# Kernel optimization log

Measured on AMD Instinct MI355X. Metric: run time of the kernel, lower is better.

Reference implementation:

```python
import jax, jax.numpy as jnp
import numpy as np

VOCAB = 100      # input_size == output_size
H = 2048         # hidden_size
NL = 2           # n_layers
SW = 256         # stack_width
SD = 200         # stack_depth
RIN = H + SW     # rnn_input_size (has_stack=True)


def _p(key, shape, fan_in):
    return jax.random.normal(key, shape, jnp.float32) / np.float32(np.sqrt(fan_in))


def setup_inputs() -> dict:
    key = jax.random.key(0)
    ks = jax.random.split(key, 12)
    return dict(
        inp=jax.random.randint(ks[0], (1,), 0, VOCAB),
        hidden=jax.random.normal(ks[1], (NL, 1, H), jnp.float32),
        stack=jax.random.normal(ks[2], (1, SD, SW), jnp.float32),
        emb=_p(ks[3], (VOCAB, H), H),
        Wc=_p(ks[4], (3, NL * H), NL * H), bc=jnp.zeros((3,), jnp.float32),
        Ws=_p(ks[5], (SW, NL * H), NL * H), bs=jnp.zeros((SW,), jnp.float32),
        Wih0=_p(ks[6], (3 * H, RIN), RIN), Whh0=_p(ks[7], (3 * H, H), H),
        bih0=jnp.zeros((3 * H,), jnp.float32), bhh0=jnp.zeros((3 * H,), jnp.float32),
        Wih1=_p(ks[8], (3 * H, H), H), Whh1=_p(ks[9], (3 * H, H), H),
        bih1=jnp.zeros((3 * H,), jnp.float32), bhh1=jnp.zeros((3 * H,), jnp.float32),
        Wd=_p(ks[10], (VOCAB, H), H), bd=jnp.zeros((VOCAB,), jnp.float32),
    )


def _gru_step(x, h, Wih, Whh, bih, bhh):
    # PyTorch GRU cell semantics. x: (1, in), h: (1, H)
    gi = x @ Wih.T + bih            # (1, 3H)
    gh = h @ Whh.T + bhh            # (1, 3H)
    i_r, i_z, i_n = jnp.split(gi, 3, axis=-1)
    h_r, h_z, h_n = jnp.split(gh, 3, axis=-1)
    r = jax.nn.sigmoid(i_r + h_r)
    z = jax.nn.sigmoid(i_z + h_z)
    n = jnp.tanh(i_n + r * h_n)
    return (1.0 - z) * n + z * h


def reference(inp, hidden, stack, emb, Wc, bc, Ws, bs,
              Wih0, Whh0, bih0, bhh0, Wih1, Whh1, bih1, bhh1, Wd, bd):
    # embedding: (1,) -> (1, 1, H)
    x_emb = emb[inp].reshape(1, 1, H)
    # hidden -> (1, NL*H) for stack control / stack input layers
    h2s = jnp.transpose(hidden, (1, 0, 2)).reshape(1, NL * H)
    controls = jax.nn.softmax(h2s @ Wc.T + bc, axis=1)      # (1, 3)
    s_in = jnp.tanh(h2s @ Ws.T + bs).reshape(1, 1, SW)      # (1, 1, SW)
    a_push = controls[0, 0]
    a_pop = controls[0, 1]
    a_noop = controls[0, 2]
    stack_up = jnp.concatenate([s_in, stack[:, :-1]], axis=1)
    stack_down = jnp.concatenate(
        [stack[:, 1:], jnp.zeros((1, 1, SW), stack.dtype)], axis=1)
    new_stack = a_noop * stack + a_push * stack_up + a_pop * stack_down
    # rnn input: concat embedding with stack top -> (1, H+SW)
    x = jnp.concatenate([x_emb, new_stack[:, :1, :]], axis=2)[0]
    h0 = _gru_step(x, hidden[0], Wih0, Whh0, bih0, bhh0)
    h1 = _gru_step(h0, hidden[1], Wih1, Whh1, bih1, bhh1)
    next_hidden = jnp.stack([h0, h1], axis=0)               # (NL, 1, H)
    logits = h1 @ Wd.T + bd                                 # (1, VOCAB)
    return logits, next_hidden, new_stack
```

## Files before the change

### kernel.cpp

```cpp
#include <hip/hip_runtime.h>
#include <hip/hip_bf16.h>

#define H 2048
#define RIN 2304
#define SW 256
#define SD 200

#define WS_CDOT 0
#define WS_SDOT 4
#define WS_GH0  260
#define WS_GH1  6404
#define WS_GI0  12548


typedef __attribute__((ext_vector_type(4))) float f32x4;

__device__ __forceinline__ float wave_reduce(float acc) {
  #pragma unroll
  for (int off = 32; off > 0; off >>= 1) acc += __shfl_down(acc, off);
  return acc;
}

__device__ __forceinline__ float dot2048_part(const float* __restrict__ w,
                                              const float* __restrict__ x) {
  int lane = threadIdx.x & 63;
  const f32x4* w4 = (const f32x4*)w + lane;
  const f32x4* x4 = (const f32x4*)x + lane;
  f32x4 a0 = w4[0],   a1 = w4[64],  a2 = w4[128], a3 = w4[192];
  f32x4 a4 = w4[256], a5 = w4[320], a6 = w4[384], a7 = w4[448];
  f32x4 b0 = x4[0],   b1 = x4[64],  b2 = x4[128], b3 = x4[192];
  f32x4 b4 = x4[256], b5 = x4[320], b6 = x4[384], b7 = x4[448];
  asm volatile("" : "+v"(a0), "+v"(a1), "+v"(a2), "+v"(a3),
                    "+v"(a4), "+v"(a5), "+v"(a6), "+v"(a7),
                    "+v"(b0), "+v"(b1), "+v"(b2), "+v"(b3),
                    "+v"(b4), "+v"(b5), "+v"(b6), "+v"(b7));
  f32x4 s = a0 * b0;
  s += a1 * b1; s += a2 * b2; s += a3 * b3;
  s += a4 * b4; s += a5 * b5; s += a6 * b6; s += a7 * b7;
  return s[0] + s[1] + s[2] + s[3];
}

__device__ __forceinline__ float sigmoidf(float x) {
  return 1.f / (1.f + expf(-x));
}

__global__ __launch_bounds__(256, 4)
void k1_matvecs(const float* __restrict__ hidden, const int* __restrict__ inp,
                const float* __restrict__ emb,
                const float* __restrict__ Wc, const float* __restrict__ bc,
                const float* __restrict__ Ws, const float* __restrict__ bs,
                const float* __restrict__ Wih0, const float* __restrict__ bih0,
                const float* __restrict__ Whh0, const float* __restrict__ bhh0,
                const float* __restrict__ Whh1, const float* __restrict__ bhh1,
                float* __restrict__ ws) {
  int w = blockIdx.x * 4 + (threadIdx.x >> 6);
  int lane = threadIdx.x & 63;
  if (w < 6144) {
    float d = wave_reduce(dot2048_part(Whh0 + (size_t)w * H, hidden));
    if (lane == 0) ws[WS_GH0 + w] = d + bhh0[w];
  } else if (w < 12288) {
    int r = w - 6144;
    float d = wave_reduce(dot2048_part(Whh1 + (size_t)r * H, hidden + H));
    if (lane == 0) ws[WS_GH1 + r] = d + bhh1[r];
  } else if (w < 18432) {
    int r = w - 12288;
    const float* erow = emb + (size_t)inp[0] * H;
    float d = wave_reduce(dot2048_part(Wih0 + (size_t)r * RIN, erow));
    if (lane == 0) ws[WS_GI0 + r] = d + bih0[r];
  } else if (w < 18435) {
    int r = w - 18432;
    const float* wr = Wc + (size_t)r * (2 * H);
    float d = wave_reduce(dot2048_part(wr, hidden) +
                          dot2048_part(wr + H, hidden + H));
    if (lane == 0) ws[WS_CDOT + r] = d + bc[r];
  } else if (w < 18691) {
    int r = w - 18435;
    const float* wr = Ws + (size_t)r * (2 * H);
    float d = wave_reduce(dot2048_part(wr, hidden) +
                          dot2048_part(wr + H, hidden + H));
    if (lane == 0) ws[WS_SDOT + r] = d + bs[r];
  }
}

__global__ __launch_bounds__(256)
void k2_stack_gru0(const float* __restrict__ stack,
                   const float* __restrict__ hidden,
                   const float* __restrict__ Wih0,
                   const float* __restrict__ ws,
                   float* out) {
  int t = threadIdx.x;
  float c0 = ws[WS_CDOT + 0], c1 = ws[WS_CDOT + 1], c2 = ws[WS_CDOT + 2];
  float m = fmaxf(c0, fmaxf(c1, c2));
  float e0 = expf(c0 - m), e1 = expf(c1 - m), e2 = expf(c2 - m);
  float inv = 1.f / (e0 + e1 + e2);
  float a_push = e0 * inv, a_pop = e1 * inv, a_noop = e2 * inv;

  int b = blockIdx.x;
  if (b >= 2048) {
    int r = b - 2048;
    float up = (r == 0) ? tanhf(ws[WS_SDOT + t]) : stack[(r - 1) * SW + t];
    float down = (r == SD - 1) ? 0.f : stack[(r + 1) * SW + t];
    out[4196 + r * SW + t] = a_noop * stack[r * SW + t] + a_push * up + a_pop * down;
    return;
  }
  __shared__ float st[SW];
  __shared__ float gred[3];
  st[t] = a_noop * stack[t] + a_push * tanhf(ws[WS_SDOT + t]) + a_pop * stack[SW + t];
  __syncthreads();
  int wv = t >> 6, lane = t & 63;
  int j = b;
  if (wv < 3) {
    const f32x4* w4 = (const f32x4*)(Wih0 + (size_t)(wv * H + j) * RIN + H);
    const f32x4* s4 = (const f32x4*)st;
    f32x4 a = w4[lane];
    f32x4 xv = s4[lane];
    f32x4 p = a * xv;
    float acc = wave_reduce(p[0] + p[1] + p[2] + p[3]);
    if (lane == 0) gred[wv] = acc;
  }
  __syncthreads();
  if (t == 0) {
    float gr = ws[WS_GI0 + j] + gred[0] + ws[WS_GH0 + j];
    float gz = ws[WS_GI0 + H + j] + gred[1] + ws[WS_GH0 + H + j];
    float r = sigmoidf(gr);
    float z = sigmoidf(gz);
    float n = tanhf(ws[WS_GI0 + 2 * H + j] + gred[2] + r * ws[WS_GH0 + 2 * H + j]);
    out[100 + j] = (1.f - z) * n + z * hidden[j];
  }
}

__global__ __launch_bounds__(192, 4)
void k3_gru1(const float* __restrict__ hidden,
             const float* __restrict__ Wih1, const float* __restrict__ bih1,
             const float* __restrict__ ws,
             float* out) {
  int j = blockIdx.x;
  int t = threadIdx.x, wv = t >> 6, lane = t & 63;
  const float* h0 = out + 100;
  __shared__ float gred[3];
  int row = wv * H + j;
  float d = wave_reduce(dot2048_part(Wih1 + (size_t)row * H, h0));
  if (lane == 0) gred[wv] = d + bih1[row];
  __syncthreads();
  if (t == 0) {
    float r = sigmoidf(gred[0] + ws[WS_GH1 + j]);
    float z = sigmoidf(gred[1] + ws[WS_GH1 + H + j]);
    float n = tanhf(gred[2] + r * ws[WS_GH1 + 2 * H + j]);
    out[100 + H + j] = (1.f - z) * n + z * hidden[H + j];
  }
}

__global__ __launch_bounds__(256, 4)
void k4_logits(const float* __restrict__ Wd, const float* __restrict__ bd,
               float* out) {
  int w = blockIdx.x * 4 + (threadIdx.x >> 6);
  int lane = threadIdx.x & 63;
  if (w >= 100) return;
  const float* h1 = out + 100 + H;
  float d = wave_reduce(dot2048_part(Wd + (size_t)w * H, h1));
  if (lane == 0) out[w] = d + bd[w];
}

extern "C" void kernel_launch(void* const* d_in, const int* in_sizes, int n_in,
                              void* d_out, int out_size, void* d_ws, size_t ws_size,
                              hipStream_t stream) {
  const int*   inp    = (const int*)d_in[0];
  const float* hidden = (const float*)d_in[1];
  const float* stack  = (const float*)d_in[2];
  const float* emb    = (const float*)d_in[3];
  const float* Wc     = (const float*)d_in[4];
  const float* bc     = (const float*)d_in[5];
  const float* Ws     = (const float*)d_in[6];
  const float* bs     = (const float*)d_in[7];
  const float* Wih0   = (const float*)d_in[8];
  const float* Whh0   = (const float*)d_in[9];
  const float* bih0   = (const float*)d_in[10];
  const float* bhh0   = (const float*)d_in[11];
  const float* Wih1   = (const float*)d_in[12];
  const float* Whh1   = (const float*)d_in[13];
  const float* bih1   = (const float*)d_in[14];
  const float* bhh1   = (const float*)d_in[15];
  const float* Wd     = (const float*)d_in[16];
  const float* bd     = (const float*)d_in[17];
  float* ws  = (float*)d_ws;
  float* out = (float*)d_out;

  k1_matvecs<<<4673, 256, 0, stream>>>(hidden, inp, emb, Wc, bc, Ws, bs,
                                       Wih0, bih0, Whh0, bhh0, Whh1, bhh1, ws);
  k2_stack_gru0<<<2248, 256, 0, stream>>>(stack, hidden, Wih0, ws, out);
  k3_gru1<<<2048, 192, 0, stream>>>(hidden, Wih1, bih1, ws, out);
  k4_logits<<<25, 256, 0, stream>>>(Wd, bd, out);
}
```

Baseline: 45.10 us.

## Process multiple matrix rows per wave with software-pipelined loads

Replaces the one-row-per-wave fully unrolled dot product with a templated routine that computes 4 (or 3) rows per wave, reusing each x chunk across rows and double-buffering the next chunk's loads. Grid sizes shrink accordingly. k3 now computes all three gate rows for one output in a single wave, which removes the shared-memory reduction and the block barrier. The aim is fewer waves, less redundant x traffic and better memory-level parallelism, at the cost of fewer loads in flight per row and lower total wave count for these memory-bound matvecs.

```diff
diff --git a/kernel.cpp b/kernel.cpp
--- a/kernel.cpp
+++ b/kernel.cpp
@@ -21,30 +21,44 @@
   return acc;
 }
 
-__device__ __forceinline__ float dot2048_part(const float* __restrict__ w,
-                                              const float* __restrict__ x) {
-  int lane = threadIdx.x & 63;
-  const f32x4* w4 = (const f32x4*)w + lane;
-  const f32x4* x4 = (const f32x4*)x + lane;
-  f32x4 a0 = w4[0],   a1 = w4[64],  a2 = w4[128], a3 = w4[192];
-  f32x4 a4 = w4[256], a5 = w4[320], a6 = w4[384], a7 = w4[448];
-  f32x4 b0 = x4[0],   b1 = x4[64],  b2 = x4[128], b3 = x4[192];
-  f32x4 b4 = x4[256], b5 = x4[320], b6 = x4[384], b7 = x4[448];
-  asm volatile("" : "+v"(a0), "+v"(a1), "+v"(a2), "+v"(a3),
-                    "+v"(a4), "+v"(a5), "+v"(a6), "+v"(a7),
-                    "+v"(b0), "+v"(b1), "+v"(b2), "+v"(b3),
-                    "+v"(b4), "+v"(b5), "+v"(b6), "+v"(b7));
-  f32x4 s = a0 * b0;
-  s += a1 * b1; s += a2 * b2; s += a3 * b3;
-  s += a4 * b4; s += a5 * b5; s += a6 * b6; s += a7 * b7;
-  return s[0] + s[1] + s[2] + s[3];
-}
-
 __device__ __forceinline__ float sigmoidf(float x) {
   return 1.f / (1.f + expf(-x));
 }
 
-__global__ __launch_bounds__(256, 4)
+template <int R>
+__device__ __forceinline__ void dot_rows(const float* __restrict__ W, size_t ldw,
+                                         const float* __restrict__ x, int nchunk,
+                                         float* part) {
+  int lane = threadIdx.x & 63;
+  const f32x4* x4 = (const f32x4*)x;
+  const f32x4* wp[R];
+  f32x4 acc[R], a[R];
+  #pragma unroll
+  for (int r = 0; r < R; ++r) {
+    wp[r] = (const f32x4*)(W + (size_t)r * ldw);
+    acc[r] = (f32x4)(0.f);
+  }
+  f32x4 xb = x4[lane];
+  #pragma unroll
+  for (int r = 0; r < R; ++r) a[r] = wp[r][lane];
+  for (int k = 1; k < nchunk; ++k) {
+    f32x4 xn = x4[k * 64 + lane];
+    f32x4 an[R];
+    #pragma unroll
+    for (int r = 0; r < R; ++r) an[r] = wp[r][k * 64 + lane];
+    #pragma unroll
+    for (int r = 0; r < R; ++r) acc[r] += a[r] * xb;
+    xb = xn;
+    #pragma unroll
+    for (int r = 0; r < R; ++r) a[r] = an[r];
+  }
+  #pragma unroll
+  for (int r = 0; r < R; ++r) acc[r] += a[r] * xb;
+  #pragma unroll
+  for (int r = 0; r < R; ++r) part[r] = acc[r][0] + acc[r][1] + acc[r][2] + acc[r][3];
+}
+
+__global__ __launch_bounds__(256)
 void k1_matvecs(const float* __restrict__ hidden, const int* __restrict__ inp,
                 const float* __restrict__ emb,
                 const float* __restrict__ Wc, const float* __restrict__ bc,
@@ -55,30 +69,48 @@
                 float* __restrict__ ws) {
   int w = blockIdx.x * 4 + (threadIdx.x >> 6);
   int lane = threadIdx.x & 63;
-  if (w < 6144) {
-    float d = wave_reduce(dot2048_part(Whh0 + (size_t)w * H, hidden));
-    if (lane == 0) ws[WS_GH0 + w] = d + bhh0[w];
-  } else if (w < 12288) {
-    int r = w - 6144;
-    float d = wave_reduce(dot2048_part(Whh1 + (size_t)r * H, hidden + H));
-    if (lane == 0) ws[WS_GH1 + r] = d + bhh1[r];
-  } else if (w < 18432) {
-    int r = w - 12288;
+  if (w > 4672) return;
+  float part[4];
+  if (w < 1536) {
+    int row = w * 4;
+    dot_rows<4>(Whh0 + (size_t)row * H, H, hidden, 8, part);
+    #pragma unroll
+    for (int r = 0; r < 4; ++r) {
+      float d = wave_reduce(part[r]);
+      if (lane == 0) ws[WS_GH0 + row + r] = d + bhh0[row + r];
+    }
+  } else if (w < 3072) {
+    int row = (w - 1536) * 4;
+    dot_rows<4>(Whh1 + (size_t)row * H, H, hidden + H, 8, part);
+    #pragma unroll
+    for (int r = 0; r < 4; ++r) {
+      float d = wave_reduce(part[r]);
+      if (lane == 0) ws[WS_GH1 + row + r] = d + bhh1[row + r];
+    }
+  } else if (w < 4608) {
+    int row = (w - 3072) * 4;
     const float* erow = emb + (size_t)inp[0] * H;
-    float d = wave_reduce(dot2048_part(Wih0 + (size_t)r * RIN, erow));
-    if (lane == 0) ws[WS_GI0 + r] = d + bih0[r];
-  } else if (w < 18435) {
-    int r = w - 18432;
-    const float* wr = Wc + (size_t)r * (2 * H);
-    float d = wave_reduce(dot2048_part(wr, hidden) +
-                          dot2048_part(wr + H, hidden + H));
-    if (lane == 0) ws[WS_CDOT + r] = d + bc[r];
-  } else if (w < 18691) {
-    int r = w - 18435;
-    const float* wr = Ws + (size_t)r * (2 * H);
-    float d = wave_reduce(dot2048_part(wr, hidden) +
-                          dot2048_part(wr + H, hidden + H));
-    if (lane == 0) ws[WS_SDOT + r] = d + bs[r];
+    dot_rows<4>(Wih0 + (size_t)row * RIN, RIN, erow, 8, part);
+    #pragma unroll
+    for (int r = 0; r < 4; ++r) {
+      float d = wave_reduce(part[r]);
+      if (lane == 0) ws[WS_GI0 + row + r] = d + bih0[row + r];
+    }
+  } else if (w < 4672) {
+    int row = (w - 4608) * 4;
+    dot_rows<4>(Ws + (size_t)row * (2 * H), 2 * H, hidden, 16, part);
+    #pragma unroll
+    for (int r = 0; r < 4; ++r) {
+      float d = wave_reduce(part[r]);
+      if (lane == 0) ws[WS_SDOT + row + r] = d + bs[r + row];
+    }
+  } else {
+    dot_rows<3>(Wc, 2 * H, hidden, 16, part);
+    #pragma unroll
+    for (int r = 0; r < 3; ++r) {
+      float d = wave_reduce(part[r]);
+      if (lane == 0) ws[WS_CDOT + r] = d + bc[r];
+    }
   }
 }
 
@@ -129,36 +161,43 @@
   }
 }
 
-__global__ __launch_bounds__(192, 4)
+__global__ __launch_bounds__(256)
 void k3_gru1(const float* __restrict__ hidden,
              const float* __restrict__ Wih1, const float* __restrict__ bih1,
              const float* __restrict__ ws,
              float* out) {
-  int j = blockIdx.x;
-  int t = threadIdx.x, wv = t >> 6, lane = t & 63;
+  int j = blockIdx.x * 4 + (threadIdx.x >> 6);
+  int lane = threadIdx.x & 63;
+  if (j >= H) return;
   const float* h0 = out + 100;
-  __shared__ float gred[3];
-  int row = wv * H + j;
-  float d = wave_reduce(dot2048_part(Wih1 + (size_t)row * H, h0));
-  if (lane == 0) gred[wv] = d + bih1[row];
-  __syncthreads();
-  if (t == 0) {
-    float r = sigmoidf(gred[0] + ws[WS_GH1 + j]);
-    float z = sigmoidf(gred[1] + ws[WS_GH1 + H + j]);
-    float n = tanhf(gred[2] + r * ws[WS_GH1 + 2 * H + j]);
+  float part[3];
+  dot_rows<3>(Wih1 + (size_t)j * H, (size_t)H * H, h0, 8, part);
+  float pr = wave_reduce(part[0]);
+  float pz = wave_reduce(part[1]);
+  float pn = wave_reduce(part[2]);
+  if (lane == 0) {
+    float r = sigmoidf(pr + bih1[j] + ws[WS_GH1 + j]);
+    float z = sigmoidf(pz + bih1[H + j] + ws[WS_GH1 + H + j]);
+    float n = tanhf(pn + bih1[2 * H + j] + r * ws[WS_GH1 + 2 * H + j]);
     out[100 + H + j] = (1.f - z) * n + z * hidden[H + j];
   }
 }
 
-__global__ __launch_bounds__(256, 4)
+__global__ __launch_bounds__(256)
 void k4_logits(const float* __restrict__ Wd, const float* __restrict__ bd,
                float* out) {
   int w = blockIdx.x * 4 + (threadIdx.x >> 6);
   int lane = threadIdx.x & 63;
-  if (w >= 100) return;
+  if (w >= 25) return;
   const float* h1 = out + 100 + H;
-  float d = wave_reduce(dot2048_part(Wd + (size_t)w * H, h1));
-  if (lane == 0) out[w] = d + bd[w];
+  int row = w * 4;
+  float part[4];
+  dot_rows<4>(Wd + (size_t)row * H, H, h1, 8, part);
+  #pragma unroll
+  for (int r = 0; r < 4; ++r) {
+    float d = wave_reduce(part[r]);
+    if (lane == 0) out[row + r] = d + bd[row + r];
+  }
 }
 
 extern "C" void kernel_launch(void* const* d_in, const int* in_sizes, int n_in,
@@ -185,9 +224,9 @@
   float* ws  = (float*)d_ws;
   float* out = (float*)d_out;
 
-  k1_matvecs<<<4673, 256, 0, stream>>>(hidden, inp, emb, Wc, bc, Ws, bs,
+  k1_matvecs<<<1169, 256, 0, stream>>>(hidden, inp, emb, Wc, bc, Ws, bs,
                                        Wih0, bih0, Whh0, bhh0, Whh1, bhh1, ws);
   k2_stack_gru0<<<2248, 256, 0, stream>>>(stack, hidden, Wih0, ws, out);
-  k3_gru1<<<2048, 192, 0, stream>>>(hidden, Wih1, bih1, ws, out);
-  k4_logits<<<25, 256, 0, stream>>>(Wd, bd, out);
-}
+  k3_gru1<<<512, 256, 0, stream>>>(hidden, Wih1, bih1, ws, out);
+  k4_logits<<<7, 256, 0, stream>>>(Wd, bd, out);
+}
```

Result: slower. 48.87 us (+8.4%).

## Stage input vectors in LDS and process multiple rows per wave in matvec kernels

Applied to the files above, without the earlier changes.

Replaces the per-wave dot product, which read both weights and input vector from global memory, with a loop-based row_dot that reads the input vector from LDS once staged per block. Each wave now handles two rows (eight rows per block), cutting the grid sizes of k1, k3 and k4. k3 now has each wave compute all three gates for its hidden unit directly, removing the shared-memory gate reduction and the block sync. Fewer waves in flight and a looped, less-unrolled weight load may reduce memory-level parallelism on this bandwidth-bound matvec.

```diff
diff --git a/kernel.cpp b/kernel.cpp
--- a/kernel.cpp
+++ b/kernel.cpp
@@ -21,30 +21,29 @@
   return acc;
 }
 
-__device__ __forceinline__ float dot2048_part(const float* __restrict__ w,
-                                              const float* __restrict__ x) {
-  int lane = threadIdx.x & 63;
-  const f32x4* w4 = (const f32x4*)w + lane;
-  const f32x4* x4 = (const f32x4*)x + lane;
-  f32x4 a0 = w4[0],   a1 = w4[64],  a2 = w4[128], a3 = w4[192];
-  f32x4 a4 = w4[256], a5 = w4[320], a6 = w4[384], a7 = w4[448];
-  f32x4 b0 = x4[0],   b1 = x4[64],  b2 = x4[128], b3 = x4[192];
-  f32x4 b4 = x4[256], b5 = x4[320], b6 = x4[384], b7 = x4[448];
-  asm volatile("" : "+v"(a0), "+v"(a1), "+v"(a2), "+v"(a3),
-                    "+v"(a4), "+v"(a5), "+v"(a6), "+v"(a7),
-                    "+v"(b0), "+v"(b1), "+v"(b2), "+v"(b3),
-                    "+v"(b4), "+v"(b5), "+v"(b6), "+v"(b7));
-  f32x4 s = a0 * b0;
-  s += a1 * b1; s += a2 * b2; s += a3 * b3;
-  s += a4 * b4; s += a5 * b5; s += a6 * b6; s += a7 * b7;
-  return s[0] + s[1] + s[2] + s[3];
-}
-
 __device__ __forceinline__ float sigmoidf(float x) {
   return 1.f / (1.f + expf(-x));
 }
 
-__global__ __launch_bounds__(256, 4)
+__device__ __forceinline__ float row_dot(const float* __restrict__ Wrow,
+                                         const f32x4* xl, int nch) {
+  int lane = threadIdx.x & 63;
+  const f32x4* w4 = (const f32x4*)Wrow + lane;
+  const f32x4* x4 = xl + lane;
+  f32x4 acc = (f32x4)(0.f);
+  for (int g = 0; g < nch; g += 4) {
+    f32x4 a0 = w4[g * 64], a1 = w4[g * 64 + 64];
+    f32x4 a2 = w4[g * 64 + 128], a3 = w4[g * 64 + 192];
+    asm volatile("" : "+v"(a0), "+v"(a1), "+v"(a2), "+v"(a3));
+    acc += a0 * x4[g * 64];
+    acc += a1 * x4[g * 64 + 64];
+    acc += a2 * x4[g * 64 + 128];
+    acc += a3 * x4[g * 64 + 192];
+  }
+  return acc[0] + acc[1] + acc[2] + acc[3];
+}
+
+__global__ __launch_bounds__(256)
 void k1_matvecs(const float* __restrict__ hidden, const int* __restrict__ inp,
                 const float* __restrict__ emb,
                 const float* __restrict__ Wc, const float* __restrict__ bc,
@@ -53,32 +52,42 @@
                 const float* __restrict__ Whh0, const float* __restrict__ bhh0,
                 const float* __restrict__ Whh1, const float* __restrict__ bhh1,
                 float* __restrict__ ws) {
-  int w = blockIdx.x * 4 + (threadIdx.x >> 6);
-  int lane = threadIdx.x & 63;
-  if (w < 6144) {
-    float d = wave_reduce(dot2048_part(Whh0 + (size_t)w * H, hidden));
-    if (lane == 0) ws[WS_GH0 + w] = d + bhh0[w];
-  } else if (w < 12288) {
-    int r = w - 6144;
-    float d = wave_reduce(dot2048_part(Whh1 + (size_t)r * H, hidden + H));
-    if (lane == 0) ws[WS_GH1 + r] = d + bhh1[r];
-  } else if (w < 18432) {
-    int r = w - 12288;
-    const float* erow = emb + (size_t)inp[0] * H;
-    float d = wave_reduce(dot2048_part(Wih0 + (size_t)r * RIN, erow));
-    if (lane == 0) ws[WS_GI0 + r] = d + bih0[r];
-  } else if (w < 18435) {
-    int r = w - 18432;
-    const float* wr = Wc + (size_t)r * (2 * H);
-    float d = wave_reduce(dot2048_part(wr, hidden) +
-                          dot2048_part(wr + H, hidden + H));
-    if (lane == 0) ws[WS_CDOT + r] = d + bc[r];
-  } else if (w < 18691) {
-    int r = w - 18435;
-    const float* wr = Ws + (size_t)r * (2 * H);
-    float d = wave_reduce(dot2048_part(wr, hidden) +
-                          dot2048_part(wr + H, hidden + H));
-    if (lane == 0) ws[WS_SDOT + r] = d + bs[r];
+  __shared__ f32x4 xl[1024];
+  int pb = blockIdx.x;
+  int t = threadIdx.x, wv = t >> 6, lane = t & 63;
+
+  const float* W; const float* x; const float* bias; float* dst;
+  int base, nch, K4, nrows;
+  size_t ld;
+  if (pb < 768) {
+    W = Whh0; x = hidden;     bias = bhh0; dst = ws + WS_GH0;
+    base = pb * 8;            nch = 8;  K4 = 512;  nrows = 8; ld = H;
+  } else if (pb < 1536) {
+    W = Whh1; x = hidden + H; bias = bhh1; dst = ws + WS_GH1;
+    base = (pb - 768) * 8;    nch = 8;  K4 = 512;  nrows = 8; ld = H;
+  } else if (pb < 2304) {
+    W = Wih0; x = emb + (size_t)inp[0] * H; bias = bih0; dst = ws + WS_GI0;
+    base = (pb - 1536) * 8;   nch = 8;  K4 = 512;  nrows = 8; ld = RIN;
+  } else if (pb < 2336) {
+    W = Ws; x = hidden;       bias = bs;  dst = ws + WS_SDOT;
+    base = (pb - 2304) * 8;   nch = 16; K4 = 1024; nrows = 8; ld = 2 * H;
+  } else {
+    W = Wc; x = hidden;       bias = bc;  dst = ws + WS_CDOT;
+    base = 0;                 nch = 16; K4 = 1024; nrows = 3; ld = 2 * H;
+  }
+
+  const f32x4* xg = (const f32x4*)x;
+  for (int i = t; i < K4; i += 256) xl[i] = xg[i];
+  __syncthreads();
+
+  #pragma unroll
+  for (int rr = 0; rr < 2; ++rr) {
+    int r = wv * 2 + rr;
+    if (r >= nrows) break;
+    int row = base + r;
+    float d = row_dot(W + (size_t)row * ld, xl, nch);
+    d = wave_reduce(d);
+    if (lane == 0) dst[row] = d + bias[row];
   }
 }
 
@@ -129,36 +138,57 @@
   }
 }
 
-__global__ __launch_bounds__(192, 4)
+__global__ __launch_bounds__(256)
 void k3_gru1(const float* __restrict__ hidden,
              const float* __restrict__ Wih1, const float* __restrict__ bih1,
              const float* __restrict__ ws,
              float* out) {
-  int j = blockIdx.x;
+  __shared__ f32x4 xl[512];
+  int pb = blockIdx.x;
   int t = threadIdx.x, wv = t >> 6, lane = t & 63;
   const float* h0 = out + 100;
-  __shared__ float gred[3];
-  int row = wv * H + j;
-  float d = wave_reduce(dot2048_part(Wih1 + (size_t)row * H, h0));
-  if (lane == 0) gred[wv] = d + bih1[row];
-  __syncthreads();
-  if (t == 0) {
-    float r = sigmoidf(gred[0] + ws[WS_GH1 + j]);
-    float z = sigmoidf(gred[1] + ws[WS_GH1 + H + j]);
-    float n = tanhf(gred[2] + r * ws[WS_GH1 + 2 * H + j]);
-    out[100 + H + j] = (1.f - z) * n + z * hidden[H + j];
-  }
-}
-
-__global__ __launch_bounds__(256, 4)
+  const f32x4* h04 = (const f32x4*)h0;
+  for (int i = t; i < 512; i += 256) xl[i] = h04[i];
+  __syncthreads();
+
+  #pragma unroll
+  for (int jj = 0; jj < 2; ++jj) {
+    int j = pb * 8 + wv * 2 + jj;
+    if (j >= H) break;
+    float dr = row_dot(Wih1 + (size_t)j * H, xl, 8);
+    float dz = row_dot(Wih1 + (size_t)(H + j) * H, xl, 8);
+    float dn = row_dot(Wih1 + (size_t)(2 * H + j) * H, xl, 8);
+    dr = wave_reduce(dr);
+    dz = wave_reduce(dz);
+    dn = wave_reduce(dn);
+    if (lane == 0) {
+      float r = sigmoidf(dr + bih1[j] + ws[WS_GH1 + j]);
+      float z = sigmoidf(dz + bih1[H + j] + ws[WS_GH1 + H + j]);
+      float n = tanhf(dn + bih1[2 * H + j] + r * ws[WS_GH1 + 2 * H + j]);
+      out[100 + H + j] = (1.f - z) * n + z * hidden[H + j];
+    }
+  }
+}
+
+__global__ __launch_bounds__(256)
 void k4_logits(const float* __restrict__ Wd, const float* __restrict__ bd,
                float* out) {
-  int w = blockIdx.x * 4 + (threadIdx.x >> 6);
-  int lane = threadIdx.x & 63;
-  if (w >= 100) return;
+  __shared__ f32x4 xl[512];
+  int pb = blockIdx.x;
+  int t = threadIdx.x, wv = t >> 6, lane = t & 63;
   const float* h1 = out + 100 + H;
-  float d = wave_reduce(dot2048_part(Wd + (size_t)w * H, h1));
-  if (lane == 0) out[w] = d + bd[w];
+  const f32x4* h14 = (const f32x4*)h1;
+  for (int i = t; i < 512; i += 256) xl[i] = h14[i];
+  __syncthreads();
+
+  #pragma unroll
+  for (int rr = 0; rr < 2; ++rr) {
+    int row = pb * 8 + wv * 2 + rr;
+    if (row >= 100) break;
+    float d = row_dot(Wd + (size_t)row * H, xl, 8);
+    d = wave_reduce(d);
+    if (lane == 0) out[row] = d + bd[row];
+  }
 }
 
 extern "C" void kernel_launch(void* const* d_in, const int* in_sizes, int n_in,
@@ -185,9 +215,9 @@
   float* ws  = (float*)d_ws;
   float* out = (float*)d_out;
 
-  k1_matvecs<<<4673, 256, 0, stream>>>(hidden, inp, emb, Wc, bc, Ws, bs,
+  k1_matvecs<<<2337, 256, 0, stream>>>(hidden, inp, emb, Wc, bc, Ws, bs,
                                        Wih0, bih0, Whh0, bhh0, Whh1, bhh1, ws);
   k2_stack_gru0<<<2248, 256, 0, stream>>>(stack, hidden, Wih0, ws, out);
-  k3_gru1<<<2048, 192, 0, stream>>>(hidden, Wih1, bih1, ws, out);
-  k4_logits<<<25, 256, 0, stream>>>(Wd, bd, out);
-}
+  k3_gru1<<<256, 256, 0, stream>>>(hidden, Wih1, bih1, ws, out);
+  k4_logits<<<13, 256, 0, stream>>>(Wd, bd, out);
+}
```

Result: slower. 49.73 us (+10.3%).
